# Kernel optimization log

Measured on AMD Instinct MI355X. Metric: run time of the kernel, lower is better.

Reference implementation:

```python
import jax, jax.numpy as jnp
import numpy as np

B, S, HID = 4, 4096, 1024
H, D = 16, 64  # num_head, attn_dim
EPS = 1e-6


def setup_inputs() -> dict:
    key = jax.random.key(0)
    ks = jax.random.split(key, 9)
    sc = 1.0 / np.sqrt(HID)
    return {
        "x": jax.random.normal(ks[0], (B, S, HID), jnp.float32),
        "Wq": jax.random.normal(ks[1], (HID, H * D), jnp.float32) * sc,
        "bq": jnp.zeros((H * D,), jnp.float32),
        "Wk": jax.random.normal(ks[2], (HID, H * D), jnp.float32) * sc,
        "bk": jnp.zeros((H * D,), jnp.float32),
        "Wv": jax.random.normal(ks[3], (HID, H * D), jnp.float32) * sc,
        "bv": jnp.zeros((H * D,), jnp.float32),
        "Wo": jax.random.normal(ks[4], (H * D, HID), jnp.float32) * sc,
        "bo": jnp.zeros((HID,), jnp.float32),
    }


def _phi(x):
    # feature_map == 'elu': elu(x) + 1
    return jax.nn.elu(x) + 1.0


def reference(x, Wq, bq, Wk, bk, Wv, bv, Wo, bo):
    bs, n, _ = x.shape
    # projections -> [b, n, h, d], then scan axis first -> [n, b, h, d]
    Q = _phi((x @ Wq + bq).reshape(bs, n, H, D)).transpose(1, 0, 2, 3)
    K = _phi((x @ Wk + bk).reshape(bs, n, H, D)).transpose(1, 0, 2, 3)
    V = (x @ Wv + bv).reshape(bs, n, H, D).transpose(1, 0, 2, 3)

    KV0 = jnp.zeros((bs, H, D, D), x.dtype)
    Ks0 = jnp.zeros((bs, H, D), x.dtype)

    def step(carry, qkv):
        KV, Ks = carry
        qi, ki, vi = qkv  # each [b, h, d]
        KV = KV + jnp.einsum('bhd,bhe->bhde', ki, vi)
        Ks = Ks + ki
        num = jnp.einsum('bhd,bhde->bhe', qi, KV)
        den = jnp.einsum('bhd,bhd->bh', qi, Ks)
        return (KV, Ks), num / (den[..., None] + EPS)

    _, out = jax.lax.scan(step, (KV0, Ks0), (Q, K, V))  # out: [n, b, h, d]
    out = out.transpose(1, 0, 2, 3).reshape(bs, n, H * D)
    return out @ Wo + bo
```

## Files before the change

### kernel.cpp

```cpp
#include <hip/hip_runtime.h>
#include <stdint.h>


#define DEVI __device__ __forceinline__

typedef __attribute__((ext_vector_type(8))) short bf16x8;
typedef __attribute__((ext_vector_type(4))) float f32x4;
typedef unsigned short u16;

DEVI u16 f2bf(float f) {
  union { float f; uint32_t u; } x; x.f = f;
  return (u16)((x.u + 0x7FFFu + ((x.u >> 16) & 1u)) >> 16);
}
DEVI float bf2f(u16 u) {
  union { uint32_t u; float f; } x; x.u = ((uint32_t)u) << 16;
  return x.f;
}
DEVI f32x4 mfma16(bf16x8 a, bf16x8 b, f32x4 c) {
  return __builtin_amdgcn_mfma_f32_16x16x32_bf16(a, b, c, 0, 0, 0);
}

typedef __attribute__((address_space(3))) void* lds_vp;
typedef const __attribute__((address_space(1))) void* glb_vp;
DEVI void gload_lds16(const void* g, void* l) {
  __builtin_amdgcn_global_load_lds((glb_vp)g, (lds_vp)l, 16, 0, 0);
}

static constexpr int Ss  = 4096;
static constexpr int Hh  = 16;
static constexpr int CC  = 64;
static constexpr int NCC = Ss / CC;

__global__ __launch_bounds__(256) void cvt_bf16_k(const float* __restrict__ in,
                                                  u16* __restrict__ out, int n8) {
  const int i = blockIdx.x * 256 + threadIdx.x;
  if (i >= n8) return;
  const float4* p = (const float4*)(in + (size_t)i * 8);
  const float4 a = p[0], b = p[1];
  union { uint4 v; u16 s[8]; } u;
  u.s[0] = f2bf(a.x); u.s[1] = f2bf(a.y); u.s[2] = f2bf(a.z); u.s[3] = f2bf(a.w);
  u.s[4] = f2bf(b.x); u.s[5] = f2bf(b.y); u.s[6] = f2bf(b.z); u.s[7] = f2bf(b.w);
  ((uint4*)out)[i] = u.v;
}

__global__ __launch_bounds__(256) void transpose_cvt_k(const float* __restrict__ in,
                                                       u16* __restrict__ out) {
  __shared__ float tl[32][33];
  const int tx = threadIdx.x & 31, ty = threadIdx.x >> 5;
  const int bx = blockIdx.x, by = blockIdx.y;
#pragma unroll
  for (int j = 0; j < 4; ++j)
    tl[ty + j * 8][tx] = in[(size_t)(by * 32 + ty + j * 8) * 1024 + bx * 32 + tx];
  __syncthreads();
#pragma unroll
  for (int j = 0; j < 4; ++j)
    out[(size_t)(bx * 32 + ty + j * 8) * 1024 + by * 32 + tx] = f2bf(tl[tx][ty + j * 8]);
}

template <bool FUSED, bool OUTF32>
__global__ __launch_bounds__(512, 2) void gemm256_k(const u16* __restrict__ A,
                                                    const u16* __restrict__ BT,
                                                    const float* __restrict__ b0,
                                                    const float* __restrict__ b1,
                                                    const float* __restrict__ b2,
                                                    void* __restrict__ out,
                                                    int M, int K) {
  __shared__ __attribute__((aligned(16))) u16 lds[65536];
  const int t = threadIdx.x, lane = t & 63, w = t >> 6;
  const int wm = w >> 2, wn = w & 3;

  const int nx = gridDim.x;
  const int nwg = nx * gridDim.y;
  const int bid = blockIdx.y * nx + blockIdx.x;
  const int swz = (bid & 7) * (nwg >> 3) + (bid >> 3);
  const int bx = swz % nx, by = swz / nx;
  const int m0 = by * 256, n0 = bx * 256;

  const u16* gA = A + (size_t)m0 * K;
  const u16* gB = BT + (size_t)n0 * K;

  const int sr  = t >> 2;
  const int sc  = (t & 3) ^ ((sr >> 1) & 3);
  auto stage = [&](const u16* gm, u16* lr, int kofs) {
    gload_lds16(gm + (size_t)sr * K + kofs + sc * 8, lr + t * 8);
    gload_lds16(gm + (size_t)(sr + 128) * K + kofs + sc * 8, lr + 4096 + t * 8);
  };

  f32x4 acc[8][4];
#pragma unroll
  for (int i = 0; i < 8; ++i)
#pragma unroll
    for (int j = 0; j < 4; ++j) acc[i][j] = f32x4{0.f, 0.f, 0.f, 0.f};

  stage(gA, lds, 0);          stage(gB, lds + 32768, 0);
  stage(gA, lds + 8192, 32);  stage(gB, lds + 40960, 32);

  const int fr = lane & 15, kq = lane >> 4;
  const int nk = K >> 6;
  for (int kt = 0; kt < nk; ++kt) {
    const int buf = kt & 1;
    u16* Ab = lds + buf * 16384;
    u16* Bb = lds + 32768 + buf * 16384;
    u16* An = lds + (buf ^ 1) * 16384;
    u16* Bn = lds + 32768 + (buf ^ 1) * 16384;
    const bool pf = (kt + 1 < nk);
    const int kon = (kt + 1) << 6;
#pragma unroll
    for (int ph = 0; ph < 2; ++ph) {
      if (pf || ph == 0) asm volatile("s_waitcnt vmcnt(4)" ::: "memory");
      else               asm volatile("s_waitcnt vmcnt(0)" ::: "memory");
      __builtin_amdgcn_s_barrier();
      asm volatile("" ::: "memory");
      if (pf) {
        stage(gA, An + ph * 8192, kon + ph * 32);
        stage(gB, Bn + ph * 8192, kon + ph * 32);
      }
      const u16* Ar = Ab + ph * 8192;
      const u16* Br = Bb + ph * 8192;
      bf16x8 af[8], bg[4];
#pragma unroll
      for (int fi = 0; fi < 8; ++fi) {
        const int row = wm * 128 + fi * 16 + fr;
        af[fi] = *(const bf16x8*)(Ar + row * 32 + ((kq ^ ((row >> 1) & 3)) << 3));
      }
#pragma unroll
      for (int fj = 0; fj < 4; ++fj) {
        const int row = wn * 64 + fj * 16 + fr;
        bg[fj] = *(const bf16x8*)(Br + row * 32 + ((kq ^ ((row >> 1) & 3)) << 3));
      }
      asm volatile("s_waitcnt lgkmcnt(0)" ::: "memory");
      __builtin_amdgcn_sched_barrier(0);
      __builtin_amdgcn_s_setprio(1);
#pragma unroll
      for (int fi = 0; fi < 8; ++fi)
#pragma unroll
        for (int fj = 0; fj < 4; ++fj)
          acc[fi][fj] = mfma16(af[fi], bg[fj], acc[fi][fj]);
      __builtin_amdgcn_s_setprio(0);
      __builtin_amdgcn_sched_barrier(0);
    }
  }

  const int rowg = (lane >> 4) * 4;
  if constexpr (!OUTF32) {
    __syncthreads();
    const int seg  = FUSED ? (n0 >> 10) : 0;
    const int lcol0 = FUSED ? (n0 & 1023) : n0;
    const float* bp = b0;
    if constexpr (FUSED) bp = (seg == 0) ? b0 : (seg == 1) ? b1 : b2;
#pragma unroll
    for (int fj = 0; fj < 4; ++fj) {
      const int col = wn * 64 + fj * 16 + fr;
      const float bv = bp[lcol0 + col];
#pragma unroll
      for (int fi = 0; fi < 8; ++fi) {
#pragma unroll
        for (int rr = 0; rr < 4; ++rr) {
          const int row = wm * 128 + fi * 16 + rowg + rr;
          float v = acc[fi][fj][rr] + bv;
          if (FUSED && seg < 2) v = (v > 0.f) ? (v + 1.f) : __expf(v);
          lds[row * 256 + (((col >> 3) ^ ((row >> 2) & 31)) << 3) + (col & 7)] = f2bf(v);
        }
      }
    }
    __syncthreads();
    u16* outp = (u16*)out + (size_t)seg * M * 1024 + (size_t)m0 * 1024 + lcol0;
#pragma unroll
    for (int it = 0; it < 16; ++it) {
      const int g = it * 512 + t;
      const int row = g >> 5, c16 = g & 31;
      const uint4 v = *(const uint4*)&lds[row * 256 + ((c16 ^ ((row >> 2) & 31)) << 3)];
      *(uint4*)(outp + (size_t)row * 1024 + c16 * 8) = v;
    }
  } else {
    float* flds = (float*)lds;
#pragma unroll
    for (int pass = 0; pass < 2; ++pass) {
      __syncthreads();
      if (wm == pass) {
#pragma unroll
        for (int fj = 0; fj < 4; ++fj) {
          const int col = wn * 64 + fj * 16 + fr;
          const float bv = b0[n0 + col];
#pragma unroll
          for (int fi = 0; fi < 8; ++fi) {
#pragma unroll
            for (int rr = 0; rr < 4; ++rr) {
              const int rl = fi * 16 + rowg + rr;
              flds[rl * 256 + (((col >> 2) ^ ((rl >> 2) & 63)) << 2) + (col & 3)] =
                  acc[fi][fj][rr] + bv;
            }
          }
        }
      }
      __syncthreads();
      float* outp = (float*)out + (size_t)(m0 + pass * 128) * 1024 + n0;
#pragma unroll
      for (int it = 0; it < 16; ++it) {
        const int g = it * 512 + t;
        const int row = g >> 6, c16 = g & 63;
        const uint4 v = *(const uint4*)&flds[row * 256 + ((c16 ^ ((row >> 2) & 63)) << 2)];
        *(uint4*)(outp + (size_t)row * 1024 + c16 * 4) = v;
      }
    }
  }
}

__global__ __launch_bounds__(256) void chunk_kv_k(const u16* __restrict__ Kb,
                                                  const u16* __restrict__ Vb,
                                                  u16* __restrict__ KVTc,
                                                  float* __restrict__ Ksc) {
  const int c = blockIdx.x, h = blockIdx.y, b = blockIdx.z;
  __shared__ u16 Kl[64][72], Vl[64][72];
  const int t = threadIdx.x;
  {
    const int i = t >> 2, c0 = (t & 3) * 16;
    const size_t g = ((size_t)(b * Ss + c * CC + i)) * 1024 + h * 64 + c0;
    const uint4* kp = (const uint4*)(Kb + g);
    uint4* kd = (uint4*)&Kl[i][c0]; kd[0] = kp[0]; kd[1] = kp[1];
    const uint4* vp = (const uint4*)(Vb + g);
    uint4* vd = (uint4*)&Vl[i][c0]; vd[0] = vp[0]; vd[1] = vp[1];
  }
  __syncthreads();
  const int e = t >> 2, d0 = (t & 3) * 16;
  float acc[16];
#pragma unroll
  for (int j = 0; j < 16; ++j) acc[j] = 0.f;
  for (int i = 0; i < 64; ++i) {
    const float v = bf2f(Vl[i][e]);
    const bf16x8 k0 = *(const bf16x8*)&Kl[i][d0];
    const bf16x8 k1 = *(const bf16x8*)&Kl[i][d0 + 8];
#pragma unroll
    for (int j = 0; j < 8; ++j) acc[j]     += v * bf2f((u16)k0[j]);
#pragma unroll
    for (int j = 0; j < 8; ++j) acc[j + 8] += v * bf2f((u16)k1[j]);
  }
  const size_t base = ((size_t)((b * Hh + h) * NCC + c)) * 4096 + (size_t)e * 64 + d0;
#pragma unroll
  for (int j = 0; j < 16; ++j) KVTc[base + j] = f2bf(acc[j]);
  if (t < 64) {
    float s = 0.f;
    for (int i = 0; i < 64; ++i) s += bf2f(Kl[i][t]);
    Ksc[((size_t)((b * Hh + h) * NCC + c)) * 64 + t] = s;
  }
}

__global__ __launch_bounds__(256) void prefix_k(const u16* __restrict__ KVTc,
                                                const float* __restrict__ Ksc,
                                                u16* __restrict__ KVpreT,
                                                float* __restrict__ Kspre) {
  const int bh = blockIdx.x, eg = blockIdx.y;
  const int t = threadIdx.x;
  float run = 0.f;
  float rk = 0.f;
  for (int c = 0; c < NCC; ++c) {
    const size_t idx = ((size_t)(bh * NCC + c)) * 4096 + (size_t)eg * 256 + t;
    KVpreT[idx] = f2bf(run);
    run += bf2f(KVTc[idx]);
    if (eg == 15 && t < 64) {
      const size_t kb = ((size_t)(bh * NCC + c)) * 64 + t;
      Kspre[kb] = rk;
      rk += Ksc[kb];
    }
  }
}

__global__ __launch_bounds__(256) void chunk_out_k(const u16* __restrict__ Qb,
                                                   const u16* __restrict__ Kb,
                                                   const u16* __restrict__ Vb,
                                                   const u16* __restrict__ KVpreT,
                                                   const float* __restrict__ Kspre,
                                                   u16* __restrict__ attn) {
  const int c = blockIdx.x, h = blockIdx.y, b = blockIdx.z;
  const int bh = b * Hh + h;
  __shared__ u16 Ql[64][72], Kl[64][72], VT[64][72], Pl[64][72];
  __shared__ float den[64];
  const int t = threadIdx.x, lane = t & 63, w = t >> 6;

  {
    const int i = t >> 2, c0 = (t & 3) * 16;
    const size_t g = ((size_t)(b * Ss + c * CC + i)) * 1024 + h * 64 + c0;
    const uint4* qp = (const uint4*)(Qb + g);
    uint4* qd = (uint4*)&Ql[i][c0]; qd[0] = qp[0]; qd[1] = qp[1];
    const uint4* kp = (const uint4*)(Kb + g);
    uint4* kd = (uint4*)&Kl[i][c0]; kd[0] = kp[0]; kd[1] = kp[1];
    const u16* vp = Vb + g;
#pragma unroll
    for (int j = 0; j < 16; ++j) VT[c0 + j][i] = vp[j];
  }
  __syncthreads();

  f32x4 sacc[4];
#pragma unroll
  for (int fj = 0; fj < 4; ++fj) sacc[fj] = f32x4{0.f, 0.f, 0.f, 0.f};
#pragma unroll
  for (int kd = 0; kd < 2; ++kd) {
    const bf16x8 aq = *(const bf16x8*)&Ql[w * 16 + (lane & 15)][kd * 32 + (lane >> 4) * 8];
#pragma unroll
    for (int fj = 0; fj < 4; ++fj) {
      const bf16x8 bk = *(const bf16x8*)&Kl[fj * 16 + (lane & 15)][kd * 32 + (lane >> 4) * 8];
      sacc[fj] = mfma16(aq, bk, sacc[fj]);
    }
  }
  float rowsum[4] = {0.f, 0.f, 0.f, 0.f};
#pragma unroll
  for (int fj = 0; fj < 4; ++fj) {
#pragma unroll
    for (int rr = 0; rr < 4; ++rr) {
      const int i_loc = w * 16 + (lane >> 4) * 4 + rr;
      const int j_loc = fj * 16 + (lane & 15);
      const float v = (j_loc <= i_loc) ? sacc[fj][rr] : 0.f;
      Pl[i_loc][j_loc] = f2bf(v);
      rowsum[rr] += v;
    }
  }
#pragma unroll
  for (int off = 1; off < 16; off <<= 1) {
#pragma unroll
    for (int rr = 0; rr < 4; ++rr) rowsum[rr] += __shfl_xor(rowsum[rr], off, 64);
  }
  if ((lane & 15) == 0) {
#pragma unroll
    for (int rr = 0; rr < 4; ++rr) den[w * 16 + (lane >> 4) * 4 + rr] = rowsum[rr];
  }
  __syncthreads();
  if (t < 64) {
    const float* ksp = Kspre + ((size_t)(bh * NCC + c)) * 64;
    float s = den[t] + 1e-6f;
    for (int d2 = 0; d2 < 64; ++d2) s += bf2f(Ql[t][d2]) * ksp[d2];
    den[t] = s;
  }
  __syncthreads();

  f32x4 oacc[4];
#pragma unroll
  for (int fj = 0; fj < 4; ++fj) oacc[fj] = f32x4{0.f, 0.f, 0.f, 0.f};
  const u16* kvb = KVpreT + ((size_t)(bh * NCC + c)) * 4096;
#pragma unroll
  for (int ks2 = 0; ks2 < 2; ++ks2) {
    const bf16x8 aq = *(const bf16x8*)&Ql[w * 16 + (lane & 15)][ks2 * 32 + (lane >> 4) * 8];
#pragma unroll
    for (int fj = 0; fj < 4; ++fj) {
      const bf16x8 bv =
          *(const bf16x8*)(kvb + (size_t)(fj * 16 + (lane & 15)) * 64 + ks2 * 32 + (lane >> 4) * 8);
      oacc[fj] = mfma16(aq, bv, oacc[fj]);
    }
  }
#pragma unroll
  for (int ks3 = 0; ks3 < 2; ++ks3) {
    const bf16x8 ap = *(const bf16x8*)&Pl[w * 16 + (lane & 15)][ks3 * 32 + (lane >> 4) * 8];
#pragma unroll
    for (int fj = 0; fj < 4; ++fj) {
      const bf16x8 bv = *(const bf16x8*)&VT[fj * 16 + (lane & 15)][ks3 * 32 + (lane >> 4) * 8];
      oacc[fj] = mfma16(ap, bv, oacc[fj]);
    }
  }
#pragma unroll
  for (int fj = 0; fj < 4; ++fj) {
#pragma unroll
    for (int rr = 0; rr < 4; ++rr) {
      const int i_loc = w * 16 + (lane >> 4) * 4 + rr;
      const int e = fj * 16 + (lane & 15);
      const float v = oacc[fj][rr] / den[i_loc];
      attn[((size_t)(b * Ss + c * CC + i_loc)) * 1024 + h * 64 + e] = f2bf(v);
    }
  }
}

extern "C" void kernel_launch(void* const* d_in, const int* in_sizes, int n_in,
                              void* d_out, int out_size, void* d_ws, size_t ws_size,
                              hipStream_t stream) {
  (void)in_sizes; (void)n_in; (void)out_size; (void)ws_size;
  const float* x  = (const float*)d_in[0];
  const float* Wq = (const float*)d_in[1];
  const float* bq = (const float*)d_in[2];
  const float* Wk = (const float*)d_in[3];
  const float* bk = (const float*)d_in[4];
  const float* Wv = (const float*)d_in[5];
  const float* bv = (const float*)d_in[6];
  const float* Wo = (const float*)d_in[7];
  const float* bo = (const float*)d_in[8];
  float* out = (float*)d_out;
  char* ws = (char*)d_ws;

  size_t off = 0;
  auto take = [&](size_t bytes) { size_t r = off; off += (bytes + 255) & ~(size_t)255; return r; };
  const size_t WQKV_B = (size_t)3072 * 1024 * 2;
  const size_t WT_B   = (size_t)1024 * 1024 * 2;
  const size_t BIG_B  = (size_t)16384 * 1024 * 2;
  const size_t KVT_B  = (size_t)64 * NCC * 4096 * 2;
  const size_t KS_B   = (size_t)64 * NCC * 64 * 4;

  u16* WqkvT  = (u16*)(ws + take(WQKV_B));
  u16* WoT    = (u16*)(ws + take(WT_B));
  size_t shared_off = take(BIG_B);
  u16* xbf    = (u16*)(ws + shared_off);
  u16* KVTc   = (u16*)(ws + shared_off);
  u16* attn   = (u16*)(ws + shared_off);
  u16* Qb     = (u16*)(ws + take(BIG_B));
  u16* Kb     = (u16*)(ws + take(BIG_B));
  u16* Vb     = (u16*)(ws + take(BIG_B));
  u16* KVpreT = (u16*)(ws + take(KVT_B));
  float* Ksc  = (float*)(ws + take(KS_B));
  float* Kspre= (float*)(ws + take(KS_B));

  const dim3 blk(256);
  cvt_bf16_k<<<dim3(8192), blk, 0, stream>>>(x, xbf, 16384 * 1024 / 8);
  const dim3 gT(32, 32);
  transpose_cvt_k<<<gT, blk, 0, stream>>>(Wq, WqkvT);
  transpose_cvt_k<<<gT, blk, 0, stream>>>(Wk, WqkvT + (size_t)1024 * 1024);
  transpose_cvt_k<<<gT, blk, 0, stream>>>(Wv, WqkvT + (size_t)2048 * 1024);
  transpose_cvt_k<<<gT, blk, 0, stream>>>(Wo, WoT);

  gemm256_k<true, false><<<dim3(12, 64), dim3(512), 0, stream>>>(
      xbf, WqkvT, bq, bk, bv, Qb, 16384, 1024);

  const dim3 gC(NCC, Hh, 4);
  chunk_kv_k<<<gC, blk, 0, stream>>>(Kb, Vb, KVTc, Ksc);
  prefix_k<<<dim3(64, 16), blk, 0, stream>>>(KVTc, Ksc, KVpreT, Kspre);
  chunk_out_k<<<gC, blk, 0, stream>>>(Qb, Kb, Vb, KVpreT, Kspre, attn);

  gemm256_k<false, true><<<dim3(4, 64), dim3(512), 0, stream>>>(
      attn, WoT, bo, NULL, NULL, out, 16384, 1024);
}
```

Measured before the change: 301.5 us.

## Use MFMA for chunk KV, vectorize prefix scan, split GEMM B-fragment loads

The per-chunk K^T V outer-product accumulation moves from scalar FMA loops to MFMA bf16 instructions on transposed LDS tiles. The prefix scan kernel now processes four elements per thread with vector loads over a quarter of the blocks. The denominator dot product in chunk_out is spread across all 256 threads with shuffle reductions instead of 64. The GEMM main loop splits B-fragment loading and staging into two halves to interleave global prefetch with MFMA work and reduce register pressure. The trade-off is scalar transposed LDS stores in chunk_kv, which may cause bank conflicts.

```diff
diff --git a/kernel.cpp b/kernel.cpp
--- a/kernel.cpp
+++ b/kernel.cpp
@@ -79,11 +79,11 @@
   const u16* gA = A + (size_t)m0 * K;
   const u16* gB = BT + (size_t)n0 * K;
 
-  const int sr  = t >> 2;
-  const int sc  = (t & 3) ^ ((sr >> 1) & 3);
-  auto stage = [&](const u16* gm, u16* lr, int kofs) {
-    gload_lds16(gm + (size_t)sr * K + kofs + sc * 8, lr + t * 8);
-    gload_lds16(gm + (size_t)(sr + 128) * K + kofs + sc * 8, lr + 4096 + t * 8);
+  const int sr = t >> 2;
+  const int sc = (t & 3) ^ ((sr >> 1) & 3);
+  auto stage = [&](const u16* gm, u16* dst, int kof) {
+    gload_lds16(gm + (size_t)sr * K + kof + sc * 8, dst + t * 8);
+    gload_lds16(gm + (size_t)(sr + 128) * K + kof + sc * 8, dst + 4096 + t * 8);
   };
 
   f32x4 acc[8][4];
@@ -96,46 +96,55 @@
   stage(gA, lds + 8192, 32);  stage(gB, lds + 40960, 32);
 
   const int fr = lane & 15, kq = lane >> 4;
+  const int rdko = ((kq ^ ((fr >> 1) & 3)) << 3);
+  const int arow0 = wm * 128 + fr;
+  const int brow0 = wn * 64 + fr;
+
   const int nk = K >> 6;
   for (int kt = 0; kt < nk; ++kt) {
     const int buf = kt & 1;
-    u16* Ab = lds + buf * 16384;
-    u16* Bb = lds + 32768 + buf * 16384;
-    u16* An = lds + (buf ^ 1) * 16384;
-    u16* Bn = lds + 32768 + (buf ^ 1) * 16384;
+    u16* Ax = lds + buf * 16384;
+    u16* Bx = lds + 32768 + buf * 16384;
+    u16* Ay = lds + (buf ^ 1) * 16384;
+    u16* By = lds + 32768 + (buf ^ 1) * 16384;
     const bool pf = (kt + 1 < nk);
     const int kon = (kt + 1) << 6;
-#pragma unroll
-    for (int ph = 0; ph < 2; ++ph) {
-      if (pf || ph == 0) asm volatile("s_waitcnt vmcnt(4)" ::: "memory");
-      else               asm volatile("s_waitcnt vmcnt(0)" ::: "memory");
+    bf16x8 af[8], bg0, bg1;
+
+#pragma unroll
+    for (int half = 0; half < 2; ++half) {
+      u16* Axh = Ax + half * 8192;
+      u16* Bxh = Bx + half * 8192;
+      if (half == 0 || pf) asm volatile("s_waitcnt vmcnt(4)" ::: "memory");
+      else                 asm volatile("s_waitcnt vmcnt(0)" ::: "memory");
       __builtin_amdgcn_s_barrier();
-      asm volatile("" ::: "memory");
-      if (pf) {
-        stage(gA, An + ph * 8192, kon + ph * 32);
-        stage(gB, Bn + ph * 8192, kon + ph * 32);
-      }
-      const u16* Ar = Ab + ph * 8192;
-      const u16* Br = Bb + ph * 8192;
-      bf16x8 af[8], bg[4];
-#pragma unroll
-      for (int fi = 0; fi < 8; ++fi) {
-        const int row = wm * 128 + fi * 16 + fr;
-        af[fi] = *(const bf16x8*)(Ar + row * 32 + ((kq ^ ((row >> 1) & 3)) << 3));
-      }
-#pragma unroll
-      for (int fj = 0; fj < 4; ++fj) {
-        const int row = wn * 64 + fj * 16 + fr;
-        bg[fj] = *(const bf16x8*)(Br + row * 32 + ((kq ^ ((row >> 1) & 3)) << 3));
-      }
+      if (pf) stage(gA, Ay + half * 8192, kon + half * 32);
+#pragma unroll
+      for (int fi = 0; fi < 8; ++fi)
+        af[fi] = *(const bf16x8*)(Axh + (arow0 + fi * 16) * 32 + rdko);
+      bg0 = *(const bf16x8*)(Bxh + brow0 * 32 + rdko);
+      bg1 = *(const bf16x8*)(Bxh + (brow0 + 16) * 32 + rdko);
       asm volatile("s_waitcnt lgkmcnt(0)" ::: "memory");
       __builtin_amdgcn_sched_barrier(0);
       __builtin_amdgcn_s_setprio(1);
 #pragma unroll
-      for (int fi = 0; fi < 8; ++fi)
-#pragma unroll
-        for (int fj = 0; fj < 4; ++fj)
-          acc[fi][fj] = mfma16(af[fi], bg[fj], acc[fi][fj]);
+      for (int fi = 0; fi < 8; ++fi) {
+        acc[fi][0] = mfma16(af[fi], bg0, acc[fi][0]);
+        acc[fi][1] = mfma16(af[fi], bg1, acc[fi][1]);
+      }
+      __builtin_amdgcn_s_setprio(0);
+      __builtin_amdgcn_sched_barrier(0);
+      if (pf) stage(gB, By + half * 8192, kon + half * 32);
+      bg0 = *(const bf16x8*)(Bxh + (brow0 + 32) * 32 + rdko);
+      bg1 = *(const bf16x8*)(Bxh + (brow0 + 48) * 32 + rdko);
+      asm volatile("s_waitcnt lgkmcnt(0)" ::: "memory");
+      __builtin_amdgcn_sched_barrier(0);
+      __builtin_amdgcn_s_setprio(1);
+#pragma unroll
+      for (int fi = 0; fi < 8; ++fi) {
+        acc[fi][2] = mfma16(af[fi], bg0, acc[fi][2]);
+        acc[fi][3] = mfma16(af[fi], bg1, acc[fi][3]);
+      }
       __builtin_amdgcn_s_setprio(0);
       __builtin_amdgcn_sched_barrier(0);
     }
@@ -211,36 +220,47 @@
                                                   u16* __restrict__ KVTc,
                                                   float* __restrict__ Ksc) {
   const int c = blockIdx.x, h = blockIdx.y, b = blockIdx.z;
-  __shared__ u16 Kl[64][72], Vl[64][72];
-  const int t = threadIdx.x;
+  __shared__ u16 KT[64][72], VT[64][72];
+  const int t = threadIdx.x, lane = t & 63, w = t >> 6;
   {
     const int i = t >> 2, c0 = (t & 3) * 16;
     const size_t g = ((size_t)(b * Ss + c * CC + i)) * 1024 + h * 64 + c0;
-    const uint4* kp = (const uint4*)(Kb + g);
-    uint4* kd = (uint4*)&Kl[i][c0]; kd[0] = kp[0]; kd[1] = kp[1];
-    const uint4* vp = (const uint4*)(Vb + g);
-    uint4* vd = (uint4*)&Vl[i][c0]; vd[0] = vp[0]; vd[1] = vp[1];
+    const u16* kp = Kb + g;
+    const u16* vp = Vb + g;
+#pragma unroll
+    for (int j = 0; j < 16; ++j) { KT[c0 + j][i] = kp[j]; VT[c0 + j][i] = vp[j]; }
   }
   __syncthreads();
-  const int e = t >> 2, d0 = (t & 3) * 16;
-  float acc[16];
-#pragma unroll
-  for (int j = 0; j < 16; ++j) acc[j] = 0.f;
-  for (int i = 0; i < 64; ++i) {
-    const float v = bf2f(Vl[i][e]);
-    const bf16x8 k0 = *(const bf16x8*)&Kl[i][d0];
-    const bf16x8 k1 = *(const bf16x8*)&Kl[i][d0 + 8];
-#pragma unroll
-    for (int j = 0; j < 8; ++j) acc[j]     += v * bf2f((u16)k0[j]);
-#pragma unroll
-    for (int j = 0; j < 8; ++j) acc[j + 8] += v * bf2f((u16)k1[j]);
-  }
-  const size_t base = ((size_t)((b * Hh + h) * NCC + c)) * 4096 + (size_t)e * 64 + d0;
-#pragma unroll
-  for (int j = 0; j < 16; ++j) KVTc[base + j] = f2bf(acc[j]);
+  f32x4 acc[4];
+#pragma unroll
+  for (int j = 0; j < 4; ++j) acc[j] = f32x4{0.f, 0.f, 0.f, 0.f};
+  const int fr = lane & 15, kq = (lane >> 4) * 8;
+#pragma unroll
+  for (int kk = 0; kk < 2; ++kk) {
+    const bf16x8 av = *(const bf16x8*)&VT[w * 16 + fr][kk * 32 + kq];
+#pragma unroll
+    for (int fj = 0; fj < 4; ++fj) {
+      const bf16x8 bk = *(const bf16x8*)&KT[fj * 16 + fr][kk * 32 + kq];
+      acc[fj] = mfma16(av, bk, acc[fj]);
+    }
+  }
+  const size_t base = ((size_t)((b * Hh + h) * NCC + c)) * 4096;
+#pragma unroll
+  for (int fj = 0; fj < 4; ++fj)
+#pragma unroll
+    for (int rr = 0; rr < 4; ++rr) {
+      const int e = w * 16 + (lane >> 4) * 4 + rr;
+      const int d = fj * 16 + fr;
+      KVTc[base + (size_t)e * 64 + d] = f2bf(acc[fj][rr]);
+    }
   if (t < 64) {
     float s = 0.f;
-    for (int i = 0; i < 64; ++i) s += bf2f(Kl[i][t]);
+#pragma unroll
+    for (int ii = 0; ii < 8; ++ii) {
+      const bf16x8 kv = *(const bf16x8*)&KT[t][ii * 8];
+#pragma unroll
+      for (int j = 0; j < 8; ++j) s += bf2f((u16)kv[j]);
+    }
     Ksc[((size_t)((b * Hh + h) * NCC + c)) * 64 + t] = s;
   }
 }
@@ -251,17 +271,20 @@
                                                 float* __restrict__ Kspre) {
   const int bh = blockIdx.x, eg = blockIdx.y;
   const int t = threadIdx.x;
-  float run = 0.f;
+  const int e4 = eg * 1024 + t * 4;
+  const u16* src = KVTc + (size_t)bh * NCC * 4096 + e4;
+  u16* dst = KVpreT + (size_t)bh * NCC * 4096 + e4;
+  const float* kss = Ksc + (size_t)bh * NCC * 64 + t;
+  float* ksd = Kspre + (size_t)bh * NCC * 64 + t;
+  float run[4] = {0.f, 0.f, 0.f, 0.f};
   float rk = 0.f;
   for (int c = 0; c < NCC; ++c) {
-    const size_t idx = ((size_t)(bh * NCC + c)) * 4096 + (size_t)eg * 256 + t;
-    KVpreT[idx] = f2bf(run);
-    run += bf2f(KVTc[idx]);
-    if (eg == 15 && t < 64) {
-      const size_t kb = ((size_t)(bh * NCC + c)) * 64 + t;
-      Kspre[kb] = rk;
-      rk += Ksc[kb];
-    }
+    union { uint2 v; u16 s[4]; } in, ov;
+    in.v = *(const uint2*)(src + (size_t)c * 4096);
+#pragma unroll
+    for (int j = 0; j < 4; ++j) { ov.s[j] = f2bf(run[j]); run[j] += bf2f(in.s[j]); }
+    *(uint2*)(dst + (size_t)c * 4096) = ov.v;
+    if (eg == 0 && t < 64) { ksd[(size_t)c * 64] = rk; rk += kss[(size_t)c * 64]; }
   }
 }
 
@@ -324,11 +347,19 @@
     for (int rr = 0; rr < 4; ++rr) den[w * 16 + (lane >> 4) * 4 + rr] = rowsum[rr];
   }
   __syncthreads();
-  if (t < 64) {
-    const float* ksp = Kspre + ((size_t)(bh * NCC + c)) * 64;
-    float s = den[t] + 1e-6f;
-    for (int d2 = 0; d2 < 64; ++d2) s += bf2f(Ql[t][d2]) * ksp[d2];
-    den[t] = s;
+  {
+    const int i = t >> 2, part = t & 3;
+    const float* ksp = Kspre + ((size_t)(bh * NCC + c)) * 64 + part * 16;
+    float s = 0.f;
+#pragma unroll
+    for (int sg = 0; sg < 2; ++sg) {
+      const bf16x8 q = *(const bf16x8*)&Ql[i][part * 16 + sg * 8];
+#pragma unroll
+      for (int j = 0; j < 8; ++j) s += bf2f((u16)q[j]) * ksp[sg * 8 + j];
+    }
+    s += __shfl_xor(s, 1, 64);
+    s += __shfl_xor(s, 2, 64);
+    if (part == 0) den[i] = den[i] + s + 1e-6f;
   }
   __syncthreads();
 
@@ -417,7 +448,7 @@
 
   const dim3 gC(NCC, Hh, 4);
   chunk_kv_k<<<gC, blk, 0, stream>>>(Kb, Vb, KVTc, Ksc);
-  prefix_k<<<dim3(64, 16), blk, 0, stream>>>(KVTc, Ksc, KVpreT, Kspre);
+  prefix_k<<<dim3(64, 4), blk, 0, stream>>>(KVTc, Ksc, KVpreT, Kspre);
   chunk_out_k<<<gC, blk, 0, stream>>>(Qb, Kb, Vb, KVpreT, Kspre, attn);
 
   gemm256_k<false, true><<<dim3(4, 64), dim3(512), 0, stream>>>(
```

Result: faster. 267.4 us (-11.3%).
